# Kernel optimization log

Hardware: AMD Instinct MI355X
Metric: run time of the kernel (lower is better)

Reference implementation:

```python
import jax, jax.numpy as jnp
import numpy as np

DIM = 1024
NUM_HEADS = 16
HEAD_DIM = DIM // NUM_HEADS
SCALE = HEAD_DIM ** -0.5


def setup_inputs() -> dict:
    key = jax.random.key(0)
    ks = jax.random.split(key, 9)
    s = DIM ** -0.5
    return {
        'x_q': jax.random.normal(ks[0], (4, 2048, DIM), dtype=jnp.float32),
        'wq': jax.random.normal(ks[1], (DIM, DIM), dtype=jnp.float32) * s,
        'bq': jax.random.normal(ks[2], (DIM,), dtype=jnp.float32) * 0.02,
        'wk': jax.random.normal(ks[3], (DIM, DIM), dtype=jnp.float32) * s,
        'bk': jax.random.normal(ks[4], (DIM,), dtype=jnp.float32) * 0.02,
        'wv': jax.random.normal(ks[5], (DIM, DIM), dtype=jnp.float32) * s,
        'bv': jax.random.normal(ks[6], (DIM,), dtype=jnp.float32) * 0.02,
        'wo': jax.random.normal(ks[7], (DIM, DIM), dtype=jnp.float32) * s,
        'bo': jax.random.normal(ks[8], (DIM,), dtype=jnp.float32) * 0.02,
    }


def reference(x_q, wq, bq, wk, bk, wv, bv, wo, bo):
    B, N, C = x_q.shape
    H, c = NUM_HEADS, HEAD_DIM
    # torch nn.Linear: y = x @ W.T + b, W is [out, in]
    q = (x_q @ wq.T + bq).reshape(B, N, H, c).transpose(0, 2, 1, 3)  # [B,H,N,c]
    k = (x_q @ wk.T + bk).reshape(B, N, H, c).transpose(0, 2, 1, 3)
    v = (x_q @ wv.T + bv).reshape(B, N, H, c).transpose(0, 2, 1, 3)
    attn = jnp.einsum('bhqc,bhkc->bhqk', q, k) * SCALE  # [B,H,N,N]
    attn = jax.nn.softmax(attn, axis=-1)
    out = jnp.einsum('bhqk,bhkc->bhqc', attn, v)  # [B,H,N,c]
    out = out.transpose(0, 2, 1, 3).reshape(B, N, C)
    return out @ wo.T + bo
```

## Files before the change

kernel.cpp:

```cpp
#include <hip/hip_runtime.h>
#include <hip/hip_bf16.h>

typedef __bf16 bf16x8 __attribute__((ext_vector_type(8)));
typedef float f32x4 __attribute__((ext_vector_type(4)));
typedef unsigned int u32x4 __attribute__((ext_vector_type(4)));

#define QSCALE 0.18033688011112042f

__device__ __forceinline__ void gload16(const void* g, void* l) {
  __builtin_amdgcn_global_load_lds(
      (const __attribute__((address_space(1))) uint32_t*)g,
      (__attribute__((address_space(3))) uint32_t*)l, 16, 0, 0);
}

__device__ __forceinline__ unsigned bf16bits(float f) {
  union { __bf16 h; unsigned short u; } c; c.h = (__bf16)f; return c.u;
}

__device__ __forceinline__ float exp2_raw(float x) {
  float r;
  asm("v_exp_f32 %0, %1" : "=v"(r) : "v"(x));
  return r;
}

__device__ __forceinline__ unsigned cvt_pk_bf16(float a, float b) {
  unsigned r;
  asm("v_cvt_pk_bf16_f32 %0, %1, %2" : "=v"(r) : "v"(a), "v"(b));
  return r;
}

#define SWAPL32(a, b) asm("v_permlane32_swap_b32 %0, %1" : "+v"(a), "+v"(b))
#define SWAPL16(a, b) asm("v_permlane16_swap_b32 %0, %1" : "+v"(a), "+v"(b))

__global__ __launch_bounds__(256) void cast_all(
    const float* __restrict__ x, const float* __restrict__ wq, const float* __restrict__ wk,
    const float* __restrict__ wv, const float* __restrict__ wo,
    __bf16* __restrict__ xbf, __bf16* __restrict__ wqb, __bf16* __restrict__ wkb,
    __bf16* __restrict__ wvb, __bf16* __restrict__ wob) {
  int b = blockIdx.x;
  const float* src;
  __bf16* dst;
  int i;
  if (b < 4096) {
    src = x; dst = xbf; i = b * 256 + threadIdx.x;
  } else {
    int s = (b - 4096) >> 9;
    i = ((b - 4096) & 511) * 256 + threadIdx.x;
    src = (s == 0) ? wq : (s == 1) ? wk : (s == 2) ? wv : wo;
    dst = (s == 0) ? wqb : (s == 1) ? wkb : (s == 2) ? wvb : wob;
  }
  const float4* p = (const float4*)src;
  float4 a = p[2 * i], c = p[2 * i + 1];
  bf16x8 v;
  v[0] = (__bf16)a.x; v[1] = (__bf16)a.y; v[2] = (__bf16)a.z; v[3] = (__bf16)a.w;
  v[4] = (__bf16)c.x; v[5] = (__bf16)c.y; v[6] = (__bf16)c.z; v[7] = (__bf16)c.w;
  ((bf16x8*)dst)[i] = v;
}

template <int MODE>
__global__ __launch_bounds__(256) void gemm_nt(
    const __bf16* __restrict__ A,
    const __bf16* __restrict__ W0, const __bf16* __restrict__ W1, const __bf16* __restrict__ W2,
    const float* __restrict__ b0, const float* __restrict__ b1, const float* __restrict__ b2,
    __bf16* __restrict__ o0, __bf16* __restrict__ o1, __bf16* __restrict__ o2,
    float* __restrict__ of) {
  __shared__ __bf16 lA[128 * 32];
  __shared__ __bf16 lB[128 * 32];
  const int t = threadIdx.x;
  const int lane = t & 63;
  const int w = t >> 6;
  const int wr = w >> 1, wc = w & 1;
  const int l16 = lane & 15, l4 = lane >> 4;
  const int m0 = blockIdx.x * 128;
  int sel, bn;
  if (MODE == 0) { sel = blockIdx.y >> 3; bn = (blockIdx.y & 7) * 128; }
  else           { sel = 0;               bn = blockIdx.y * 128; }
  const __bf16* W   = (sel == 0) ? W0 : (sel == 1) ? W1 : W2;
  const float* bias = (sel == 0) ? b0 : (sel == 1) ? b1 : b2;

  f32x4 acc[4][4] = {};

  for (int k0 = 0; k0 < 1024; k0 += 32) {
    __syncthreads();
#pragma unroll
    for (int i = 0; i < 2; i++) {
      int c = t + i * 256;
      int r = c >> 2, cp = c & 3;
      gload16(A + (size_t)(m0 + r) * 1024 + k0 + cp * 8, lA + c * 8);
      gload16(W + (size_t)(bn + r) * 1024 + k0 + cp * 8, lB + c * 8);
    }
    __syncthreads();
    bf16x8 af[4], bfr[4];
#pragma unroll
    for (int m = 0; m < 4; m++)
      af[m] = *(const bf16x8*)(lA + (wr * 64 + m * 16 + l16) * 32 + l4 * 8);
#pragma unroll
    for (int n = 0; n < 4; n++)
      bfr[n] = *(const bf16x8*)(lB + (wc * 64 + n * 16 + l16) * 32 + l4 * 8);
#pragma unroll
    for (int m = 0; m < 4; m++)
#pragma unroll
      for (int n = 0; n < 4; n++)
        acc[m][n] = __builtin_amdgcn_mfma_f32_16x16x32_bf16(af[m], bfr[n], acc[m][n], 0, 0, 0);
  }

  const float scl = (MODE == 0 && sel == 0) ? QSCALE : 1.0f;
  __bf16* outp = (sel == 0) ? o0 : (sel == 1) ? o1 : o2;
#pragma unroll
  for (int n = 0; n < 4; n++) {
    const int col = bn + wc * 64 + n * 16 + l16;
    const float bv = bias[col];
    if (MODE == 0 && sel == 2) {
      const int h = col >> 6, hc = col & 63;
#pragma unroll
      for (int m = 0; m < 4; m++) {
        const int nnb = m0 + wr * 64 + m * 16 + l4 * 4;
        const int b_ = nnb >> 11, nn = nnb & 2047;
        ushort4 ov;
        ov.x = (unsigned short)bf16bits(acc[m][n][0] + bv);
        ov.y = (unsigned short)bf16bits(acc[m][n][1] + bv);
        ov.z = (unsigned short)bf16bits(acc[m][n][2] + bv);
        ov.w = (unsigned short)bf16bits(acc[m][n][3] + bv);
        *(ushort4*)(outp + ((size_t)(b_ * 16 + h) * 64 + hc) * 2048 + nn) = ov;
      }
    } else {
#pragma unroll
      for (int m = 0; m < 4; m++) {
#pragma unroll
        for (int j = 0; j < 4; j++) {
          const int row = m0 + wr * 64 + m * 16 + l4 * 4 + j;
          float v = acc[m][n][j] + bv;
          if (MODE == 0) {
            v *= scl;
            int b_ = row >> 11, nn = row & 2047;
            int h = col >> 6, hc = col & 63;
            outp[(((size_t)(b_ * 16 + h)) * 2048 + nn) * 64 + hc] = (__bf16)v;
          } else {
            of[(size_t)row * 1024 + col] = v;
          }
        }
      }
    }
  }
}

__global__ __launch_bounds__(256) void attn_fwd(const __bf16* __restrict__ Q,
                                                const __bf16* __restrict__ K,
                                                const __bf16* __restrict__ Vt,
                                                __bf16* __restrict__ O) {
  __shared__ __bf16 sm[16384];
  const int flat = blockIdx.x;
  const int wg = (flat & 7) * 128 + (flat >> 3);
  const int bh = wg >> 4;
  const int q0 = (wg & 15) * 128;
  const __bf16* Qh = Q + (size_t)bh * 2048 * 64;
  const __bf16* Kh = K + (size_t)bh * 2048 * 64;
  const __bf16* Vh = Vt + (size_t)bh * 64 * 2048;
  const int t = threadIdx.x, lane = t & 63, w = t >> 6;
  const int l16 = lane & 15, l4 = lane >> 4;

  bf16x8 qf[2][2];
#pragma unroll
  for (int st = 0; st < 2; st++)
#pragma unroll
    for (int kk = 0; kk < 2; kk++)
      qf[st][kk] = *(const bf16x8*)(Qh + (size_t)(q0 + w * 32 + st * 16 + l16) * 64 + kk * 32 + l4 * 8);

  f32x4 ao[2][4] = {};
  f32x4 rs4[2] = {};
  bf16x8 onesf;
#pragma unroll
  for (int i = 0; i < 8; i++) onesf[i] = (__bf16)1.0f;

  const int rdbase = l4 * 512 + l16 * 8;
  const int vb = 8192 + l4 * 512 + l16 * 8;

  f32x4 sA[2][4], sB[2][4];

#pragma unroll
  for (int i = 0; i < 2; i++) {
    int ic = w * 2 + i;
    gload16(Kh + (size_t)lane * 64 + ic * 8,          sm + ic * 512 + lane * 8);
    gload16(Vh + (size_t)lane * 2048 + ic * 8,        sm + 8192 + ic * 512 + lane * 8);
    gload16(Kh + (size_t)(64 + lane) * 64 + ic * 8,   sm + 4096 + ic * 512 + lane * 8);
    gload16(Vh + (size_t)lane * 2048 + 64 + ic * 8,   sm + 12288 + ic * 512 + lane * 8);
  }
  __syncthreads();

#define QK_N(KLDS, SCUR, n)                                                    \
  {                                                                            \
    bf16x8 kf0 = *(const bf16x8*)((KLDS) + rdbase + (n) * 128);                \
    bf16x8 kf1 = *(const bf16x8*)((KLDS) + rdbase + 2048 + (n) * 128);         \
    f32x4 z = {};                                                              \
    SCUR[0][(n)] = __builtin_amdgcn_mfma_f32_16x16x32_bf16(kf0, qf[0][0], z, 0, 0, 0); \
    SCUR[1][(n)] = __builtin_amdgcn_mfma_f32_16x16x32_bf16(kf0, qf[1][0], z, 0, 0, 0); \
    SCUR[0][(n)] = __builtin_amdgcn_mfma_f32_16x16x32_bf16(kf1, qf[0][1], SCUR[0][(n)], 0, 0, 0); \
    SCUR[1][(n)] = __builtin_amdgcn_mfma_f32_16x16x32_bf16(kf1, qf[1][1], SCUR[1][(n)], 0, 0, 0); \
  }

#define SM_GROUP(SP, st_, g_)                                                  \
  {                                                                            \
    float p0 = exp2_raw(SP[(st_)][2 * (g_)][0]),     p1 = exp2_raw(SP[(st_)][2 * (g_)][1]); \
    float p2 = exp2_raw(SP[(st_)][2 * (g_)][2]),     p3 = exp2_raw(SP[(st_)][2 * (g_)][3]); \
    float p4 = exp2_raw(SP[(st_)][2 * (g_) + 1][0]), p5 = exp2_raw(SP[(st_)][2 * (g_) + 1][1]); \
    float p6 = exp2_raw(SP[(st_)][2 * (g_) + 1][2]), p7 = exp2_raw(SP[(st_)][2 * (g_) + 1][3]); \
    unsigned c00 = cvt_pk_bf16(p0, p1), c01 = cvt_pk_bf16(p2, p3);             \
    unsigned c10 = cvt_pk_bf16(p4, p5), c11 = cvt_pk_bf16(p6, p7);             \
    SWAPL32(c00, c10); SWAPL32(c01, c11);                                      \
    SWAPL16(c00, c10); SWAPL16(c01, c11);                                      \
    u32x4 tv = {c00, c01, c10, c11};                                           \
    pk[(st_)][(g_)] = tv;                                                      \
  }

#define ATTN_ITER(T, CUR, SPREV, SCUR)                                         \
  {                                                                            \
    const __bf16* vlds = sm + (CUR) * 4096;                                    \
    bf16x8 vf[2][4];                                                           \
    _Pragma("unroll")                                                          \
    for (int g = 0; g < 2; g++)                                                \
      _Pragma("unroll")                                                        \
      for (int cb = 0; cb < 4; cb++)                                           \
        vf[g][cb] = *(const bf16x8*)(vlds + vb + g * 2048 + cb * 128);         \
    __syncthreads();                                                           \
    if ((T) + 2 < 32) {                                                        \
      const int kvn = ((T) + 2) * 64;                                          \
      __bf16* dst = sm + (CUR) * 4096;                                         \
      _Pragma("unroll")                                                        \
      for (int i = 0; i < 2; i++) {                                            \
        int ic = w * 2 + i;                                                    \
        gload16(Kh + (size_t)(kvn + lane) * 64 + ic * 8, dst + ic * 512 + lane * 8); \
        gload16(Vh + (size_t)lane * 2048 + kvn + ic * 8, dst + 8192 + ic * 512 + lane * 8); \
      }                                                                        \
    }                                                                          \
    u32x4 pk[2][2];                                                            \
    __builtin_amdgcn_s_setprio(1);                                             \
    if ((T) + 1 < 32) {                                                        \
      const __bf16* klds = sm + ((CUR) ^ 1) * 4096;                            \
      _Pragma("unroll")                                                        \
      for (int n = 0; n < 4; n++) {                                            \
        QK_N(klds, SCUR, n);                                                   \
        SM_GROUP(SPREV, (n >> 1), (n & 1));                                    \
      }                                                                        \
    } else {                                                                   \
      _Pragma("unroll")                                                        \
      for (int n = 0; n < 4; n++) SM_GROUP(SPREV, (n >> 1), (n & 1));          \
    }                                                                          \
    _Pragma("unroll")                                                          \
    for (int st = 0; st < 2; st++)                                             \
      _Pragma("unroll")                                                        \
      for (int g = 0; g < 2; g++) {                                            \
        union { u32x4 u; bf16x8 h; } cv; cv.u = pk[st][g];                     \
        rs4[st] = __builtin_amdgcn_mfma_f32_16x16x32_bf16(onesf, cv.h, rs4[st], 0, 0, 0); \
        _Pragma("unroll")                                                      \
        for (int cb = 0; cb < 4; cb++)                                         \
          ao[st][cb] = __builtin_amdgcn_mfma_f32_16x16x32_bf16(vf[g][cb], cv.h, ao[st][cb], 0, 0, 0); \
      }                                                                        \
    __builtin_amdgcn_s_setprio(0);                                             \
  }

#pragma unroll
  for (int n = 0; n < 4; n++) QK_N(sm, sA, n);

  for (int tkv = 0; tkv < 32; tkv += 2) {
    ATTN_ITER(tkv,     0, sA, sB);
    ATTN_ITER(tkv + 1, 1, sB, sA);
  }
#undef ATTN_ITER
#undef SM_GROUP
#undef QK_N

  const int b_ = bh >> 4, h = bh & 15;
#pragma unroll
  for (int st = 0; st < 2; st++) {
    const float inv = 1.f / rs4[st][0];
    const int qrow = q0 + w * 32 + st * 16 + l16;
#pragma unroll
    for (int cb = 0; cb < 4; cb++) {
      ushort4 ov;
      ov.x = (unsigned short)bf16bits(ao[st][cb][0] * inv);
      ov.y = (unsigned short)bf16bits(ao[st][cb][1] * inv);
      ov.z = (unsigned short)bf16bits(ao[st][cb][2] * inv);
      ov.w = (unsigned short)bf16bits(ao[st][cb][3] * inv);
      *(ushort4*)(O + ((size_t)b_ * 2048 + qrow) * 1024 + h * 64 + cb * 16 + l4 * 4) = ov;
    }
  }
}

extern "C" void kernel_launch(void* const* d_in, const int* in_sizes, int n_in,
                              void* d_out, int out_size, void* d_ws, size_t ws_size,
                              hipStream_t stream) {
  const float* x  = (const float*)d_in[0];
  const float* wq = (const float*)d_in[1];
  const float* bq = (const float*)d_in[2];
  const float* wk = (const float*)d_in[3];
  const float* bk = (const float*)d_in[4];
  const float* wv = (const float*)d_in[5];
  const float* bv = (const float*)d_in[6];
  const float* wo = (const float*)d_in[7];
  const float* bo = (const float*)d_in[8];
  float* out = (float*)d_out;

  const size_t NX = 8388608;
  const size_t NW = 1048576;
  __bf16* xbf = (__bf16*)d_ws;
  __bf16* wqb = xbf + NX;
  __bf16* wkb = wqb + NW;
  __bf16* wvb = wkb + NW;
  __bf16* wob = wvb + NW;
  __bf16* Qb  = wob + NW;
  __bf16* Kb  = Qb + NX;
  __bf16* Vtb = Kb + NX;

  cast_all<<<6144, 256, 0, stream>>>(x, wq, wk, wv, wo, xbf, wqb, wkb, wvb, wob);

  gemm_nt<0><<<dim3(64, 24), 256, 0, stream>>>(xbf, wqb, wkb, wvb, bq, bk, bv,
                                               Qb, Kb, Vtb, nullptr);
  attn_fwd<<<1024, 256, 0, stream>>>(Qb, Kb, Vtb, xbf );
  gemm_nt<1><<<dim3(64, 8), 256, 0, stream>>>(xbf, wob, nullptr, nullptr, bo, nullptr, nullptr,
                                              nullptr, nullptr, nullptr, out);
}
```

Before: 185.3 us.

## Replace QKV projection GEMM with 256x256-tile double-buffered 8-wave kernel

Adds a dedicated QKV projection kernel that uses 256x256 output tiles, 512 threads and a 64-wide K step. Operands are double-buffered in LDS via direct global-to-LDS loads with an XOR swizzle, and the loop interleaves quarter-tile MFMA groups with staged loads and priority hints. Block indices are remapped so neighbouring blocks share tiles for better L2 reuse. The goal is higher data reuse and overlap of loads with MFMA work, at the cost of one block per CU, heavy register use (128 accumulators) and only 384 blocks across 256 CUs.

```diff
diff --git a/kernel.cpp b/kernel.cpp
--- a/kernel.cpp
+++ b/kernel.cpp
@@ -55,6 +55,165 @@
   v[0] = (__bf16)a.x; v[1] = (__bf16)a.y; v[2] = (__bf16)a.z; v[3] = (__bf16)a.w;
   v[4] = (__bf16)c.x; v[5] = (__bf16)c.y; v[6] = (__bf16)c.z; v[7] = (__bf16)c.w;
   ((bf16x8*)dst)[i] = v;
+}
+
+__global__ __launch_bounds__(512, 1) void gemm_qkv(
+    const __bf16* __restrict__ A,
+    const __bf16* __restrict__ W0, const __bf16* __restrict__ W1, const __bf16* __restrict__ W2,
+    const float* __restrict__ b0, const float* __restrict__ b1, const float* __restrict__ b2,
+    __bf16* __restrict__ o0, __bf16* __restrict__ o1, __bf16* __restrict__ o2) {
+  __shared__ __bf16 bufA[2][256 * 64];
+  __shared__ __bf16 bufB[2][256 * 64];
+  const int t = threadIdx.x;
+  const int lane = t & 63, w = t >> 6;
+  const int l16 = lane & 15, l4 = lane >> 4;
+  const int wr = w >> 2, wc = w & 3;
+
+  const int flat = blockIdx.x + 32 * blockIdx.y;
+  const int sb = (flat & 7) * 48 + (flat >> 3);
+  const int m0 = (sb & 31) * 256;
+  const int nb = sb >> 5;
+  const int sel = nb >> 2;
+  const int bn = (nb & 3) * 256;
+  const __bf16* W    = (sel == 0) ? W0 : (sel == 1) ? W1 : W2;
+  const float* bias  = (sel == 0) ? b0 : (sel == 1) ? b1 : b2;
+
+  const int exo = (((t & 7) ^ ((t >> 3) & 7)) * 8);
+  const int rA  = t >> 3;
+  const int cB  = (t & 255) >> 3;
+  const int bB  = t >> 8;
+  const int c7  = (t & 7) * 8;
+  const int xf  = (l16 & 7) << 3;
+
+#define STAGE_A(bi, h, ke)                                                      \
+  { _Pragma("unroll") for (int j_ = 0; j_ < 2; j_++) {                          \
+      int row_ = j_ * 128 + (h) * 64 + rA;                                      \
+      gload16(A + (size_t)(m0 + row_) * 1024 + (ke) + exo,                      \
+              &bufA[bi][row_ * 64 + c7]); } }
+#define STAGE_B(bi, h, ke)                                                      \
+  { _Pragma("unroll") for (int j_ = 0; j_ < 2; j_++) {                          \
+      int row_ = (bB + 2 * j_) * 64 + (h) * 32 + cB;                            \
+      gload16(W + (size_t)(bn + row_) * 1024 + (ke) + exo,                      \
+              &bufB[bi][row_ * 64 + c7]); } }
+#define LOADA(bi, qm)                                                           \
+  _Pragma("unroll") for (int mm = 0; mm < 4; mm++)                              \
+    _Pragma("unroll") for (int kk = 0; kk < 2; kk++)                            \
+      a[mm][kk] = *(const bf16x8*)(&bufA[bi][(wr * 128 + (qm) * 64 + mm * 16 + l16) * 64 + ((kk * 32 + l4 * 8) ^ xf)]);
+#define LOADB(bi, qn, B_)                                                       \
+  _Pragma("unroll") for (int nn = 0; nn < 2; nn++)                              \
+    _Pragma("unroll") for (int kk = 0; kk < 2; kk++)                            \
+      B_[nn][kk] = *(const bf16x8*)(&bufB[bi][(wc * 64 + (qn) * 32 + nn * 16 + l16) * 64 + ((kk * 32 + l4 * 8) ^ xf)]);
+#define MFMA_Q(qm, qn, B_)                                                      \
+  { __builtin_amdgcn_s_setprio(1);                                              \
+    _Pragma("unroll") for (int mm = 0; mm < 4; mm++)                            \
+      _Pragma("unroll") for (int nn = 0; nn < 2; nn++)                          \
+        _Pragma("unroll") for (int kk = 0; kk < 2; kk++)                        \
+          acc[(qm) * 4 + mm][(qn) * 2 + nn] = __builtin_amdgcn_mfma_f32_16x16x32_bf16( \
+              a[mm][kk], B_[nn][kk], acc[(qm) * 4 + mm][(qn) * 2 + nn], 0, 0, 0); \
+    __builtin_amdgcn_s_setprio(0); }
+#define BAR __builtin_amdgcn_s_barrier()
+#define WAIT_LGKM { asm volatile("s_waitcnt lgkmcnt(0)" ::: "memory"); __builtin_amdgcn_sched_barrier(0); }
+#define WAIT_VM(n) { asm volatile("s_waitcnt vmcnt(" #n ")" ::: "memory"); }
+
+  f32x4 acc[8][4] = {};
+  bf16x8 a[4][2], bq0[2][2], bq1[2][2];
+
+  STAGE_A(0, 0, 0);
+  STAGE_B(0, 0, 0);
+  STAGE_B(0, 1, 0);
+  STAGE_A(0, 1, 0);
+  STAGE_A(1, 0, 64);
+  STAGE_B(1, 0, 64);
+  STAGE_B(1, 1, 64);
+  WAIT_VM(6);
+  BAR;
+
+#define ITER(i, LASTF)                                                          \
+  {                                                                             \
+    const int kO  = (2 * (i) + 1) * 64;                                         \
+    const int kE2 = (2 * (i) + 2) * 64;                                         \
+    const int kO2 = (2 * (i) + 3) * 64;                                         \
+                                     \
+    LOADA(0, 0); LOADB(0, 0, bq0);                                              \
+    STAGE_A(1, 1, kO);                                                          \
+    BAR; WAIT_LGKM; MFMA_Q(0, 0, bq0); BAR;                                     \
+                                                                \
+    LOADB(0, 1, bq1);                                                           \
+    if (!(LASTF)) STAGE_A(0, 0, kE2);                                           \
+    BAR; WAIT_LGKM; MFMA_Q(0, 1, bq1); BAR;                                     \
+                                                                \
+    LOADA(0, 1);                                                                \
+    if (!(LASTF)) STAGE_B(0, 0, kE2);                                           \
+    BAR; WAIT_LGKM; MFMA_Q(1, 1, bq1); BAR;                                     \
+                                                  \
+    if (!(LASTF)) STAGE_B(0, 1, kE2);                                           \
+    BAR; WAIT_LGKM; MFMA_Q(1, 0, bq0);                                          \
+    if (LASTF) { WAIT_VM(0); } else { WAIT_VM(6); }                             \
+    BAR;                                                                        \
+                                               \
+    LOADA(1, 0); LOADB(1, 0, bq0);                                              \
+    if (!(LASTF)) STAGE_A(0, 1, kE2);                                           \
+    BAR; WAIT_LGKM; MFMA_Q(0, 0, bq0); BAR;                                     \
+                                                                \
+    LOADB(1, 1, bq1);                                                           \
+    if (!(LASTF)) STAGE_A(1, 0, kO2);                                           \
+    BAR; WAIT_LGKM; MFMA_Q(0, 1, bq1); BAR;                                     \
+                                                                \
+    LOADA(1, 1);                                                                \
+    if (!(LASTF)) STAGE_B(1, 0, kO2);                                           \
+    BAR; WAIT_LGKM; MFMA_Q(1, 1, bq1); BAR;                                     \
+                                                  \
+    if (!(LASTF)) STAGE_B(1, 1, kO2);                                           \
+    BAR; WAIT_LGKM; MFMA_Q(1, 0, bq0);                                          \
+    if (!(LASTF)) { WAIT_VM(6); }                                               \
+    BAR;                                                                        \
+  }
+
+  for (int i = 0; i < 7; ++i) ITER(i, 0);
+  ITER(7, 1);
+#undef ITER
+
+#pragma unroll
+  for (int ni = 0; ni < 4; ni++) {
+    const int col = bn + wc * 64 + ni * 16 + l16;
+    const float bv = bias[col];
+    if (sel == 2) {
+      const int h = col >> 6, hc = col & 63;
+#pragma unroll
+      for (int mi = 0; mi < 8; mi++) {
+        const int nnb = m0 + wr * 128 + mi * 16 + l4 * 4;
+        const int b_ = nnb >> 11, nn = nnb & 2047;
+        ushort4 ov;
+        ov.x = (unsigned short)bf16bits(acc[mi][ni][0] + bv);
+        ov.y = (unsigned short)bf16bits(acc[mi][ni][1] + bv);
+        ov.z = (unsigned short)bf16bits(acc[mi][ni][2] + bv);
+        ov.w = (unsigned short)bf16bits(acc[mi][ni][3] + bv);
+        *(ushort4*)(o2 + ((size_t)(b_ * 16 + h) * 64 + hc) * 2048 + nn) = ov;
+      }
+    } else {
+      const float scl = (sel == 0) ? QSCALE : 1.0f;
+      __bf16* outp = (sel == 0) ? o0 : o1;
+      const int h = col >> 6, hc = col & 63;
+#pragma unroll
+      for (int mi = 0; mi < 8; mi++) {
+#pragma unroll
+        for (int j = 0; j < 4; j++) {
+          const int row = m0 + wr * 128 + mi * 16 + l4 * 4 + j;
+          float v = (acc[mi][ni][j] + bv) * scl;
+          const int b_ = row >> 11, nn = row & 2047;
+          outp[(((size_t)(b_ * 16 + h)) * 2048 + nn) * 64 + hc] = (__bf16)v;
+        }
+      }
+    }
+  }
+#undef STAGE_A
+#undef STAGE_B
+#undef LOADA
+#undef LOADB
+#undef MFMA_Q
+#undef BAR
+#undef WAIT_LGKM
+#undef WAIT_VM
 }
 
 template <int MODE>
@@ -313,8 +472,8 @@
 
   cast_all<<<6144, 256, 0, stream>>>(x, wq, wk, wv, wo, xbf, wqb, wkb, wvb, wob);
 
-  gemm_nt<0><<<dim3(64, 24), 256, 0, stream>>>(xbf, wqb, wkb, wvb, bq, bk, bv,
-                                               Qb, Kb, Vtb, nullptr);
+  gemm_qkv<<<dim3(32, 12), 512, 0, stream>>>(xbf, wqb, wkb, wvb, bq, bk, bv,
+                                             Qb, Kb, Vtb);
   attn_fwd<<<1024, 256, 0, stream>>>(Qb, Kb, Vtb, xbf );
   gemm_nt<1><<<dim3(64, 8), 256, 0, stream>>>(xbf, wob, nullptr, nullptr, bo, nullptr, nullptr,
                                               nullptr, nullptr, nullptr, out);
```

Measured after the change: 196.4 us. +6.0%, slower.
